# Kernel tuning notes

Hardware: AMD Instinct MI355X
Metric: run time of the kernel (lower is better)

Reference implementation:

```python
import jax, jax.numpy as jnp
import numpy as np

N_S, N_T, E = 50000, 50000, 600000
D_IN, D_H, D_OUT = 256, 128, 64


def setup_inputs() -> dict:
    key = jax.random.key(0)
    k1, k2, k3, k4, k5, k6 = jax.random.split(key, 6)
    edge_src = jax.random.randint(k1, (E,), 0, N_S, dtype=jnp.int32)
    edge_dst = jax.random.randint(k2, (E,), 0, N_T, dtype=jnp.int32)
    edge_index = jnp.stack([edge_src, edge_dst], axis=0)  # [2, E]
    x_s = jax.random.normal(k3, (N_S, D_IN), dtype=jnp.float32)
    x_t = jax.random.normal(k4, (N_T, D_IN), dtype=jnp.float32)
    W0 = jax.random.normal(k5, (D_IN, D_H), dtype=jnp.float32) * (1.0 / np.sqrt(D_IN))
    W1 = jax.random.normal(k6, (D_H, D_OUT), dtype=jnp.float32) * (1.0 / np.sqrt(D_H))
    return {"edge_index": edge_index, "x_s": x_s, "x_t": x_t, "W0": W0, "W1": W1}


def gcn_conv(x, src, dst, W):
    """PyG GCNConv, bias=False: D^{-1/2}(A+I)D^{-1/2} (x @ W)."""
    N = x.shape[0]
    h = x @ W  # [N, out]
    loops = jnp.arange(N, dtype=src.dtype)
    s = jnp.concatenate([src, loops])  # add self-loops
    d = jnp.concatenate([dst, loops])
    deg = jax.ops.segment_sum(jnp.ones_like(d, dtype=h.dtype), d, num_segments=N)
    dinv = jnp.where(deg > 0, jax.lax.rsqrt(deg), 0.0)
    norm = dinv[s] * dinv[d]  # [E+N]
    return jax.ops.segment_sum(h[s] * norm[:, None], d, num_segments=N)


def reference(edge_index, x_s, x_t, W0, W1):
    n_s = x_s.shape[0]
    src = edge_index[0]
    dst = edge_index[1] + n_s  # targets live in the x_t block
    acts = [jax.nn.relu, lambda v: v]
    Ws = [W0, W1]
    for W, act in zip(Ws, acts):
        x = jnp.concatenate([x_s, x_t], axis=0)
        x = act(gcn_conv(x, src, dst, W))
        x_s, x_t = x[:n_s], x[n_s:]
    return (x_s, x_t)
```

## Files before the change

kernel.cpp:

```cpp
#include <hip/hip_runtime.h>
#include <cstdint>
#include <cstddef>

typedef unsigned short u16;
typedef unsigned int   u32;
typedef __attribute__((ext_vector_type(8))) short bf16x8;
typedef __attribute__((ext_vector_type(4))) float f32x4;

#define D_IN  256
#define D_H   128
#define D_OUT 64
#define LSTR  72

__device__ __forceinline__ float bf2f(u16 u){
  union { u32 i; float f; } v; v.i = ((u32)u) << 16; return v.f;
}
__device__ __forceinline__ u16 f2bf(float f){
  union { float f; u32 i; } v; v.f = f;
  u32 r = (v.i + 0x7fffu + ((v.i >> 16) & 1u)) >> 16;
  return (u16)r;
}

__global__ void k_wprep(const float* __restrict__ W0, const float* __restrict__ W1,
                        u16* __restrict__ W0t, u16* __restrict__ W1t,
                        int* __restrict__ deg, int n_t){
  int i = blockIdx.x * 256 + threadIdx.x;
  if (i < 128 * 256){
    int n = i >> 8, k = i & 255;
    W0t[i] = f2bf(W0[(size_t)k * 128 + n]);
  } else if (i < 128 * 256 + 64 * 128){
    int j = i - 128 * 256;
    int n = j >> 7, k = j & 127;
    W1t[j] = f2bf(W1[(size_t)k * 64 + n]);
  } else if (i - (128 * 256 + 64 * 128) < n_t){
    deg[i - (128 * 256 + 64 * 128)] = 0;
  }
}

__global__ void k_deg(const int* __restrict__ dst, int E, int* __restrict__ deg){
  int e = blockIdx.x * 256 + threadIdx.x;
  if (e < E) atomicAdd(&deg[dst[e]], 1);
}

__global__ __launch_bounds__(256) void k_bsum(const int* __restrict__ deg, int N,
                                              int* __restrict__ bsum){
  __shared__ int s[256];
  int tid = threadIdx.x;
  int i = blockIdx.x * 256 + tid;
  s[tid] = (i < N) ? deg[i] : 0;
  __syncthreads();
  for (int o = 128; o > 0; o >>= 1){
    if (tid < o) s[tid] += s[tid + o];
    __syncthreads();
  }
  if (tid == 0) bsum[blockIdx.x] = s[0];
}

__global__ __launch_bounds__(256) void k_off(const int* __restrict__ deg, int N,
                                             const int* __restrict__ bsum, int nb,
                                             int* __restrict__ off, int* __restrict__ cursor,
                                             float* __restrict__ dinv){
  __shared__ int s[256];
  __shared__ int sbase[256];
  const int tid = threadIdx.x;
  const int bid = blockIdx.x;
  const int i   = bid * 256 + tid;
  int acc = 0;
  for (int j = tid; j < bid; j += 256) acc += bsum[j];
  sbase[tid] = acc;
  int v = (i < N) ? deg[i] : 0;
  s[tid] = v;
  __syncthreads();
  for (int o = 128; o > 0; o >>= 1){
    if (tid < o) sbase[tid] += sbase[tid + o];
    __syncthreads();
  }
  for (int o = 1; o < 256; o <<= 1){
    int t = (tid >= o) ? s[tid - o] : 0;
    __syncthreads();
    s[tid] += t;
    __syncthreads();
  }
  if (i < N){
    int excl = s[tid] - v + sbase[0];
    off[i] = excl;
    cursor[i] = excl;
    dinv[i] = rsqrtf((float)v + 1.0f);
  }
}

__global__ void k_fill(const int* __restrict__ src, const int* __restrict__ dst,
                       int E, int* __restrict__ cursor, int* __restrict__ csr){
  int e = blockIdx.x * 256 + threadIdx.x;
  if (e < E){
    int d = dst[e];
    int p = atomicAdd(&cursor[d], 1);
    csr[p] = src[e];
  }
}

__global__ __launch_bounds__(256) void k_gemm1(
    const float* __restrict__ Xs, const float* __restrict__ Xt,
    const u16* __restrict__ W0t, int M, int n_s,
    u16* __restrict__ out)
{
  __shared__ u16 As[128 * LSTR];
  __shared__ u16 Bs[128 * LSTR];
  const int t    = threadIdx.x;
  const int wave = t >> 6, lane = t & 63;
  const int wm   = (wave >> 1) * 64, wn = (wave & 1) * 64;
  const int lm   = lane & 15, quad = lane >> 4;
  const int row0 = blockIdx.x * 128;

  f32x4 acc[4][4];
  const f32x4 z = {0.f, 0.f, 0.f, 0.f};
  #pragma unroll
  for (int i = 0; i < 4; i++)
    #pragma unroll
    for (int j = 0; j < 4; j++) acc[i][j] = z;

  const int ar = t >> 1;
  const int kh = (t & 1) * 32;
  const int r  = row0 + ar;
  const float* xp = nullptr;
  if (r < M) xp = (r < n_s) ? (Xs + (size_t)r * D_IN) : (Xt + (size_t)(r - n_s) * D_IN);
  const u16* wrow = W0t + (size_t)ar * D_IN + kh;

  float4 a4[8];
  int4   b4[4];
  if (xp){
    #pragma unroll
    for (int j = 0; j < 8; j++) a4[j] = *(const float4*)(xp + kh + j * 4);
  } else {
    float4 zz = make_float4(0,0,0,0);
    #pragma unroll
    for (int j = 0; j < 8; j++) a4[j] = zz;
  }
  #pragma unroll
  for (int j = 0; j < 4; j++) b4[j] = *(const int4*)(wrow + j * 8);

  for (int k0 = 0; k0 < D_IN; k0 += 64){
    __syncthreads();
    {
      u16 abuf[32];
      #pragma unroll
      for (int j = 0; j < 8; j++){
        abuf[j*4+0] = f2bf(a4[j].x); abuf[j*4+1] = f2bf(a4[j].y);
        abuf[j*4+2] = f2bf(a4[j].z); abuf[j*4+3] = f2bf(a4[j].w);
      }
      u16* ap = &As[ar * LSTR + kh];
      *(int4*)(ap +  0) = *(int4*)&abuf[0];
      *(int4*)(ap +  8) = *(int4*)&abuf[8];
      *(int4*)(ap + 16) = *(int4*)&abuf[16];
      *(int4*)(ap + 24) = *(int4*)&abuf[24];
      u16* bp = &Bs[ar * LSTR + kh];
      *(int4*)(bp +  0) = b4[0];
      *(int4*)(bp +  8) = b4[1];
      *(int4*)(bp + 16) = b4[2];
      *(int4*)(bp + 24) = b4[3];
    }
    __syncthreads();

    if (k0 + 64 < D_IN){
      if (xp){
        #pragma unroll
        for (int j = 0; j < 8; j++) a4[j] = *(const float4*)(xp + k0 + 64 + kh + j * 4);
      }
      #pragma unroll
      for (int j = 0; j < 4; j++) b4[j] = *(const int4*)(wrow + k0 + 64 + j * 8);
    }

    #pragma unroll
    for (int kk = 0; kk < 64; kk += 32){
      bf16x8 af[4], bfr[4];
      #pragma unroll
      for (int i = 0; i < 4; i++)
        af[i] = *(const bf16x8*)&As[(wm + i*16 + lm) * LSTR + kk + quad*8];
      #pragma unroll
      for (int i = 0; i < 4; i++)
        bfr[i] = *(const bf16x8*)&Bs[(wn + i*16 + lm) * LSTR + kk + quad*8];
      #pragma unroll
      for (int mi = 0; mi < 4; mi++)
        #pragma unroll
        for (int ni = 0; ni < 4; ni++)
          acc[mi][ni] = __builtin_amdgcn_mfma_f32_16x16x32_bf16(
              af[mi], bfr[ni], acc[mi][ni], 0, 0, 0);
    }
  }

  #pragma unroll
  for (int mi = 0; mi < 4; mi++){
    int rbase = row0 + wm + mi * 16 + quad * 4;
    #pragma unroll
    for (int rr = 0; rr < 4; rr++){
      int m = rbase + rr;
      if (m >= M) continue;
      u16* op = out + (size_t)m * D_H + wn + lm;
      #pragma unroll
      for (int ni = 0; ni < 4; ni++)
        op[ni * 16] = f2bf(acc[mi][ni][rr]);
    }
  }
}

__global__ __launch_bounds__(256) void k_aggf(
    const int* __restrict__ off, const int* __restrict__ deg,
    const int* __restrict__ csr, const float* __restrict__ dinv,
    u16* __restrict__ h1, int n_s, int n_t)
{
  int w    = (blockIdx.x * 256 + threadIdx.x) >> 6;
  int lane = threadIdx.x & 63;
  if (w >= n_t) return;
  const int g = lane >> 4;
  const int c = lane & 15;
  int start = off[w];
  int n     = deg[w];

  float r[8], p[8];
  #pragma unroll
  for (int q = 0; q < 8; q++){ r[q] = 0.f; p[q] = 0.f; }

  int i = 0;
  for (; i + 8 <= n; i += 8){
    int sa = csr[start + i + g];
    int sb = csr[start + i + 4 + g];
    int4 da = *(const int4*)(h1 + (size_t)sa * D_H + c * 8);
    int4 db = *(const int4*)(h1 + (size_t)sb * D_H + c * 8);
    const u16* ha = (const u16*)&da;
    const u16* hb = (const u16*)&db;
    #pragma unroll
    for (int q = 0; q < 8; q++){
      float va = bf2f(ha[q]), vb = bf2f(hb[q]);
      r[q] += va + vb;
      p[q] += fmaxf(va, 0.f) + fmaxf(vb, 0.f);
    }
  }
  for (; i < n; i += 4){
    if (i + g < n){
      int sa = csr[start + i + g];
      int4 da = *(const int4*)(h1 + (size_t)sa * D_H + c * 8);
      const u16* ha = (const u16*)&da;
      #pragma unroll
      for (int q = 0; q < 8; q++){
        float va = bf2f(ha[q]);
        r[q] += va;
        p[q] += fmaxf(va, 0.f);
      }
    }
  }

  #pragma unroll
  for (int q = 0; q < 8; q++){
    r[q] += __shfl_xor(r[q], 16, 64);
    r[q] += __shfl_xor(r[q], 32, 64);
    p[q] += __shfl_xor(p[q], 16, 64);
    p[q] += __shfl_xor(p[q], 32, 64);
  }

  if (g == 0){
    float di  = dinv[w];
    float di2 = di * di;
    u16* selfp = h1 + (size_t)(n_s + w) * D_H + c * 8;
    int4 hs = *(const int4*)selfp;
    const u16* hh = (const u16*)&hs;
    u16 ob[8];
    #pragma unroll
    for (int q = 0; q < 8; q++){
      float zq = fmaxf(di * r[q] + di2 * bf2f(hh[q]), 0.f);
      float uq = di * p[q] + di2 * zq;
      ob[q] = f2bf(uq);
    }
    *(int4*)selfp = *(int4*)ob;
  }
}

__global__ __launch_bounds__(256) void k_gemm2(
    const u16* __restrict__ h1, const u16* __restrict__ W1t,
    int M, int n_s, float* __restrict__ out)
{
  __shared__ u16 As[128 * LSTR];
  __shared__ u16 Bs[64 * LSTR];
  const int t    = threadIdx.x;
  const int wave = t >> 6, lane = t & 63;
  const int wm   = wave * 32;
  const int lm   = lane & 15, quad = lane >> 4;
  const int row0 = blockIdx.x * 128;

  f32x4 acc[2][4];
  const f32x4 z = {0.f, 0.f, 0.f, 0.f};
  #pragma unroll
  for (int i = 0; i < 2; i++)
    #pragma unroll
    for (int j = 0; j < 4; j++) acc[i][j] = z;

  const int ar = t >> 1;
  const int kh = (t & 1) * 32;
  const int r  = row0 + ar;
  const bool relu_a = (r < n_s);
  const int bn = t >> 2;
  const int bk = (t & 3) * 16;

  int4 a4[4], w4[2];
  if (r < M){
    const u16* hp = h1 + (size_t)r * D_H + kh;
    #pragma unroll
    for (int j = 0; j < 4; j++) a4[j] = *(const int4*)(hp + j * 8);
  } else {
    int4 zz = make_int4(0,0,0,0);
    #pragma unroll
    for (int j = 0; j < 4; j++) a4[j] = zz;
  }
  w4[0] = *(const int4*)(W1t + (size_t)bn * D_H + bk);
  w4[1] = *(const int4*)(W1t + (size_t)bn * D_H + bk + 8);

  for (int k0 = 0; k0 < D_H; k0 += 64){
    __syncthreads();
    {
      u16 abuf[32];
      #pragma unroll
      for (int j = 0; j < 4; j++){
        u16* hh = (u16*)&a4[j];
        #pragma unroll
        for (int q = 0; q < 8; q++){
          u16 v = hh[q];
          abuf[j*8+q] = (relu_a && (v & 0x8000u)) ? (u16)0 : v;
        }
      }
      u16* ap = &As[ar * LSTR + kh];
      *(int4*)(ap +  0) = *(int4*)&abuf[0];
      *(int4*)(ap +  8) = *(int4*)&abuf[8];
      *(int4*)(ap + 16) = *(int4*)&abuf[16];
      *(int4*)(ap + 24) = *(int4*)&abuf[24];
      u16* bp = &Bs[bn * LSTR + bk];
      *(int4*)(bp + 0) = w4[0];
      *(int4*)(bp + 8) = w4[1];
    }
    __syncthreads();

    if (k0 + 64 < D_H){
      if (r < M){
        const u16* hp = h1 + (size_t)r * D_H + k0 + 64 + kh;
        #pragma unroll
        for (int j = 0; j < 4; j++) a4[j] = *(const int4*)(hp + j * 8);
      }
      w4[0] = *(const int4*)(W1t + (size_t)bn * D_H + k0 + 64 + bk);
      w4[1] = *(const int4*)(W1t + (size_t)bn * D_H + k0 + 64 + bk + 8);
    }

    #pragma unroll
    for (int kk = 0; kk < 64; kk += 32){
      bf16x8 af[2], bfr[4];
      #pragma unroll
      for (int i = 0; i < 2; i++)
        af[i] = *(const bf16x8*)&As[(wm + i*16 + lm) * LSTR + kk + quad*8];
      #pragma unroll
      for (int i = 0; i < 4; i++)
        bfr[i] = *(const bf16x8*)&Bs[(i*16 + lm) * LSTR + kk + quad*8];
      #pragma unroll
      for (int mi = 0; mi < 2; mi++)
        #pragma unroll
        for (int ni = 0; ni < 4; ni++)
          acc[mi][ni] = __builtin_amdgcn_mfma_f32_16x16x32_bf16(
              af[mi], bfr[ni], acc[mi][ni], 0, 0, 0);
    }
  }

  #pragma unroll
  for (int mi = 0; mi < 2; mi++){
    int rbase = row0 + wm + mi * 16 + quad * 4;
    #pragma unroll
    for (int rr = 0; rr < 4; rr++){
      int m = rbase + rr;
      if (m >= M) continue;
      float* op = out + (size_t)m * D_OUT + lm;
      #pragma unroll
      for (int ni = 0; ni < 4; ni++)
        op[ni * 16] = acc[mi][ni][rr];
    }
  }
}

static inline size_t alup(size_t x){ return (x + 255) & ~(size_t)255; }

extern "C" void kernel_launch(void* const* d_in, const int* in_sizes, int n_in,
                              void* d_out, int out_size, void* d_ws, size_t ws_size,
                              hipStream_t stream)
{
  const int*   ei = (const int*)d_in[0];
  const float* xs = (const float*)d_in[1];
  const float* xt = (const float*)d_in[2];
  const float* W0 = (const float*)d_in[3];
  const float* W1 = (const float*)d_in[4];
  const int E   = in_sizes[0] / 2;
  const int n_s = in_sizes[1] / D_IN;
  const int n_t = in_sizes[2] / D_IN;
  const int M   = n_s + n_t;
  const int* src = ei;
  const int* dst = ei + E;
  const int nb_t = (n_t + 255) / 256;

  char* p = (char*)d_ws;
  int*   deg    = (int*)p;    p += alup((size_t)n_t * 4);
  int*   off    = (int*)p;    p += alup((size_t)n_t * 4);
  int*   cursor = (int*)p;    p += alup((size_t)n_t * 4);
  float* dinv   = (float*)p;  p += alup((size_t)n_t * 4);
  int*   bsum   = (int*)p;    p += alup((size_t)nb_t * 4);
  int*   csr    = (int*)p;    p += alup((size_t)E * 4);
  u16*   W0t    = (u16*)p;    p += alup((size_t)D_H * D_IN * 2);
  u16*   W1t    = (u16*)p;    p += alup((size_t)D_OUT * D_H * 2);
  u16*   h1     = (u16*)p;    p += alup((size_t)M * D_H * 2);

  const int wprep_n = 128*256 + 64*128 + n_t;
  k_wprep <<<(wprep_n + 255) / 256, 256, 0, stream>>>(W0, W1, W0t, W1t, deg, n_t);
  k_deg   <<<(E + 255) / 256, 256, 0, stream>>>(dst, E, deg);
  k_bsum  <<<nb_t, 256, 0, stream>>>(deg, n_t, bsum);
  k_off   <<<nb_t, 256, 0, stream>>>(deg, n_t, bsum, nb_t, off, cursor, dinv);
  k_fill  <<<(E + 255) / 256, 256, 0, stream>>>(src, dst, E, cursor, csr);

  k_gemm1<<<(M + 127) / 128, 256, 0, stream>>>(xs, xt, W0t, M, n_s, h1);
  k_aggf <<<(n_t + 3) / 4, 256, 0, stream>>>(off, deg, csr, dinv, h1, n_s, n_t);
  k_gemm2<<<(M + 127) / 128, 256, 0, stream>>>(h1, W1t, M, n_s, (float*)d_out);
}
```

Before: 279.5 us.

## Drop LDS staging in both GEMMs; load MFMA fragments directly from global

Both dense GEMM kernels stop staging tiles through shared memory with __syncthreads barriers. Each wave now owns 32 rows and loads its A and B MFMA fragments straight from global memory into registers, with register double-buffering across K steps. This removes the LDS traffic and barriers, but each wave now re-reads the whole weight matrix from global or cache, and A-row loads become strided per lane rather than coalesced.

Result: no change. 280.6 us (+0.4%).

```diff
diff --git a/kernel.cpp b/kernel.cpp
--- a/kernel.cpp
+++ b/kernel.cpp
@@ -10,7 +10,6 @@
 #define D_IN  256
 #define D_H   128
 #define D_OUT 64
-#define LSTR  72
 
 __device__ __forceinline__ float bf2f(u16 u){
   union { u32 i; float f; } v; v.i = ((u32)u) << 16; return v.f;
@@ -104,101 +103,80 @@
     const u16* __restrict__ W0t, int M, int n_s,
     u16* __restrict__ out)
 {
-  __shared__ u16 As[128 * LSTR];
-  __shared__ u16 Bs[128 * LSTR];
   const int t    = threadIdx.x;
   const int wave = t >> 6, lane = t & 63;
-  const int wm   = (wave >> 1) * 64, wn = (wave & 1) * 64;
   const int lm   = lane & 15, quad = lane >> 4;
-  const int row0 = blockIdx.x * 128;
-
-  f32x4 acc[4][4];
+  const int rowW = blockIdx.x * 128 + wave * 32;
+
+  const float* pa0;
+  const float* pa1;
+  {
+    int r0 = rowW + lm;       int c0 = (r0 < M) ? r0 : 0;
+    int r1 = rowW + 16 + lm;  int c1 = (r1 < M) ? r1 : 0;
+    pa0 = ((c0 < n_s) ? (Xs + (size_t)c0 * D_IN) : (Xt + (size_t)(c0 - n_s) * D_IN)) + quad * 8;
+    pa1 = ((c1 < n_s) ? (Xs + (size_t)c1 * D_IN) : (Xt + (size_t)(c1 - n_s) * D_IN)) + quad * 8;
+  }
+  const u16* pb = W0t + (size_t)lm * D_IN + quad * 8;
+
+  f32x4 acc[2][8];
   const f32x4 z = {0.f, 0.f, 0.f, 0.f};
   #pragma unroll
-  for (int i = 0; i < 4; i++)
-    #pragma unroll
-    for (int j = 0; j < 4; j++) acc[i][j] = z;
-
-  const int ar = t >> 1;
-  const int kh = (t & 1) * 32;
-  const int r  = row0 + ar;
-  const float* xp = nullptr;
-  if (r < M) xp = (r < n_s) ? (Xs + (size_t)r * D_IN) : (Xt + (size_t)(r - n_s) * D_IN);
-  const u16* wrow = W0t + (size_t)ar * D_IN + kh;
-
-  float4 a4[8];
-  int4   b4[4];
-  if (xp){
-    #pragma unroll
-    for (int j = 0; j < 8; j++) a4[j] = *(const float4*)(xp + kh + j * 4);
-  } else {
-    float4 zz = make_float4(0,0,0,0);
-    #pragma unroll
-    for (int j = 0; j < 8; j++) a4[j] = zz;
-  }
-  #pragma unroll
-  for (int j = 0; j < 4; j++) b4[j] = *(const int4*)(wrow + j * 8);
-
-  for (int k0 = 0; k0 < D_IN; k0 += 64){
-    __syncthreads();
-    {
-      u16 abuf[32];
-      #pragma unroll
-      for (int j = 0; j < 8; j++){
-        abuf[j*4+0] = f2bf(a4[j].x); abuf[j*4+1] = f2bf(a4[j].y);
-        abuf[j*4+2] = f2bf(a4[j].z); abuf[j*4+3] = f2bf(a4[j].w);
-      }
-      u16* ap = &As[ar * LSTR + kh];
-      *(int4*)(ap +  0) = *(int4*)&abuf[0];
-      *(int4*)(ap +  8) = *(int4*)&abuf[8];
-      *(int4*)(ap + 16) = *(int4*)&abuf[16];
-      *(int4*)(ap + 24) = *(int4*)&abuf[24];
-      u16* bp = &Bs[ar * LSTR + kh];
-      *(int4*)(bp +  0) = b4[0];
-      *(int4*)(bp +  8) = b4[1];
-      *(int4*)(bp + 16) = b4[2];
-      *(int4*)(bp + 24) = b4[3];
-    }
-    __syncthreads();
-
-    if (k0 + 64 < D_IN){
-      if (xp){
-        #pragma unroll
-        for (int j = 0; j < 8; j++) a4[j] = *(const float4*)(xp + k0 + 64 + kh + j * 4);
-      }
-      #pragma unroll
-      for (int j = 0; j < 4; j++) b4[j] = *(const int4*)(wrow + k0 + 64 + j * 8);
-    }
-
-    #pragma unroll
-    for (int kk = 0; kk < 64; kk += 32){
-      bf16x8 af[4], bfr[4];
-      #pragma unroll
-      for (int i = 0; i < 4; i++)
-        af[i] = *(const bf16x8*)&As[(wm + i*16 + lm) * LSTR + kk + quad*8];
-      #pragma unroll
-      for (int i = 0; i < 4; i++)
-        bfr[i] = *(const bf16x8*)&Bs[(wn + i*16 + lm) * LSTR + kk + quad*8];
-      #pragma unroll
-      for (int mi = 0; mi < 4; mi++)
-        #pragma unroll
-        for (int ni = 0; ni < 4; ni++)
-          acc[mi][ni] = __builtin_amdgcn_mfma_f32_16x16x32_bf16(
-              af[mi], bfr[ni], acc[mi][ni], 0, 0, 0);
-    }
-  }
-
-  #pragma unroll
-  for (int mi = 0; mi < 4; mi++){
-    int rbase = row0 + wm + mi * 16 + quad * 4;
+  for (int i = 0; i < 2; i++)
+    #pragma unroll
+    for (int j = 0; j < 8; j++) acc[i][j] = z;
+
+  float4 a[2][4];
+  int4   b[2][8];
+
+  a[0][0] = *(const float4*)(pa0);
+  a[0][1] = *(const float4*)(pa0 + 4);
+  a[0][2] = *(const float4*)(pa1);
+  a[0][3] = *(const float4*)(pa1 + 4);
+  #pragma unroll
+  for (int nf = 0; nf < 8; nf++)
+    b[0][nf] = *(const int4*)(pb + (size_t)nf * 16 * D_IN);
+
+  #pragma unroll
+  for (int kk = 0; kk < 8; kk++){
+    const int cur = kk & 1, nxt = cur ^ 1;
+    if (kk < 7){
+      const int ko = (kk + 1) * 32;
+      a[nxt][0] = *(const float4*)(pa0 + ko);
+      a[nxt][1] = *(const float4*)(pa0 + ko + 4);
+      a[nxt][2] = *(const float4*)(pa1 + ko);
+      a[nxt][3] = *(const float4*)(pa1 + ko + 4);
+      #pragma unroll
+      for (int nf = 0; nf < 8; nf++)
+        b[nxt][nf] = *(const int4*)(pb + (size_t)nf * 16 * D_IN + ko);
+    }
+    bf16x8 af[2];
+    #pragma unroll
+    for (int mi = 0; mi < 2; mi++){
+      const float* fa = (const float*)&a[cur][mi * 2];
+      u16 tmp[8];
+      #pragma unroll
+      for (int q = 0; q < 8; q++) tmp[q] = f2bf(fa[q]);
+      af[mi] = *(const bf16x8*)tmp;
+    }
+    #pragma unroll
+    for (int mi = 0; mi < 2; mi++)
+      #pragma unroll
+      for (int nf = 0; nf < 8; nf++)
+        acc[mi][nf] = __builtin_amdgcn_mfma_f32_16x16x32_bf16(
+            af[mi], *(const bf16x8*)&b[cur][nf], acc[mi][nf], 0, 0, 0);
+  }
+
+  #pragma unroll
+  for (int mi = 0; mi < 2; mi++){
+    int rbase = rowW + mi * 16 + quad * 4;
     #pragma unroll
     for (int rr = 0; rr < 4; rr++){
       int m = rbase + rr;
       if (m >= M) continue;
-      u16* op = out + (size_t)m * D_H + wn + lm;
-      #pragma unroll
-      for (int ni = 0; ni < 4; ni++)
-        op[ni * 16] = f2bf(acc[mi][ni][rr]);
+      u16* op = out + (size_t)m * D_H + lm;
+      #pragma unroll
+      for (int nf = 0; nf < 8; nf++)
+        op[nf * 16] = f2bf(acc[mi][nf][rr]);
     }
   }
 }
@@ -274,17 +252,32 @@
   }
 }
 
+__device__ __forceinline__ bf16x8 relu_bf(int4 v, bool relu){
+  const u16* s = (const u16*)&v;
+  u16 tmp[8];
+  #pragma unroll
+  for (int q = 0; q < 8; q++){
+    u16 x = s[q];
+    tmp[q] = (relu && (x & 0x8000u)) ? (u16)0 : x;
+  }
+  return *(const bf16x8*)tmp;
+}
+
 __global__ __launch_bounds__(256) void k_gemm2(
     const u16* __restrict__ h1, const u16* __restrict__ W1t,
     int M, int n_s, float* __restrict__ out)
 {
-  __shared__ u16 As[128 * LSTR];
-  __shared__ u16 Bs[64 * LSTR];
   const int t    = threadIdx.x;
   const int wave = t >> 6, lane = t & 63;
-  const int wm   = wave * 32;
   const int lm   = lane & 15, quad = lane >> 4;
-  const int row0 = blockIdx.x * 128;
+  const int rowW = blockIdx.x * 128 + wave * 32;
+
+  int r0 = rowW + lm, r1 = rowW + 16 + lm;
+  const bool relu0 = (r0 < n_s), relu1 = (r1 < n_s);
+  int c0 = (r0 < M) ? r0 : 0, c1 = (r1 < M) ? r1 : 0;
+  const u16* pa0 = h1 + (size_t)c0 * D_H + quad * 8;
+  const u16* pa1 = h1 + (size_t)c1 * D_H + quad * 8;
+  const u16* pb  = W1t + (size_t)lm * D_H + quad * 8;
 
   f32x4 acc[2][4];
   const f32x4 z = {0.f, 0.f, 0.f, 0.f};
@@ -293,89 +286,46 @@
     #pragma unroll
     for (int j = 0; j < 4; j++) acc[i][j] = z;
 
-  const int ar = t >> 1;
-  const int kh = (t & 1) * 32;
-  const int r  = row0 + ar;
-  const bool relu_a = (r < n_s);
-  const int bn = t >> 2;
-  const int bk = (t & 3) * 16;
-
-  int4 a4[4], w4[2];
-  if (r < M){
-    const u16* hp = h1 + (size_t)r * D_H + kh;
-    #pragma unroll
-    for (int j = 0; j < 4; j++) a4[j] = *(const int4*)(hp + j * 8);
-  } else {
-    int4 zz = make_int4(0,0,0,0);
-    #pragma unroll
-    for (int j = 0; j < 4; j++) a4[j] = zz;
-  }
-  w4[0] = *(const int4*)(W1t + (size_t)bn * D_H + bk);
-  w4[1] = *(const int4*)(W1t + (size_t)bn * D_H + bk + 8);
-
-  for (int k0 = 0; k0 < D_H; k0 += 64){
-    __syncthreads();
-    {
-      u16 abuf[32];
-      #pragma unroll
-      for (int j = 0; j < 4; j++){
-        u16* hh = (u16*)&a4[j];
-        #pragma unroll
-        for (int q = 0; q < 8; q++){
-          u16 v = hh[q];
-          abuf[j*8+q] = (relu_a && (v & 0x8000u)) ? (u16)0 : v;
-        }
-      }
-      u16* ap = &As[ar * LSTR + kh];
-      *(int4*)(ap +  0) = *(int4*)&abuf[0];
-      *(int4*)(ap +  8) = *(int4*)&abuf[8];
-      *(int4*)(ap + 16) = *(int4*)&abuf[16];
-      *(int4*)(ap + 24) = *(int4*)&abuf[24];
-      u16* bp = &Bs[bn * LSTR + bk];
-      *(int4*)(bp + 0) = w4[0];
-      *(int4*)(bp + 8) = w4[1];
-    }
-    __syncthreads();
-
-    if (k0 + 64 < D_H){
-      if (r < M){
-        const u16* hp = h1 + (size_t)r * D_H + k0 + 64 + kh;
-        #pragma unroll
-        for (int j = 0; j < 4; j++) a4[j] = *(const int4*)(hp + j * 8);
-      }
-      w4[0] = *(const int4*)(W1t + (size_t)bn * D_H + k0 + 64 + bk);
-      w4[1] = *(const int4*)(W1t + (size_t)bn * D_H + k0 + 64 + bk + 8);
-    }
-
-    #pragma unroll
-    for (int kk = 0; kk < 64; kk += 32){
-      bf16x8 af[2], bfr[4];
-      #pragma unroll
-      for (int i = 0; i < 2; i++)
-        af[i] = *(const bf16x8*)&As[(wm + i*16 + lm) * LSTR + kk + quad*8];
-      #pragma unroll
-      for (int i = 0; i < 4; i++)
-        bfr[i] = *(const bf16x8*)&Bs[(i*16 + lm) * LSTR + kk + quad*8];
-      #pragma unroll
-      for (int mi = 0; mi < 2; mi++)
-        #pragma unroll
-        for (int ni = 0; ni < 4; ni++)
-          acc[mi][ni] = __builtin_amdgcn_mfma_f32_16x16x32_bf16(
-              af[mi], bfr[ni], acc[mi][ni], 0, 0, 0);
-    }
+  int4 a[2][2], b[2][4];
+  a[0][0] = *(const int4*)(pa0);
+  a[0][1] = *(const int4*)(pa1);
+  #pragma unroll
+  for (int nf = 0; nf < 4; nf++)
+    b[0][nf] = *(const int4*)(pb + (size_t)nf * 16 * D_H);
+
+  #pragma unroll
+  for (int kk = 0; kk < 4; kk++){
+    const int cur = kk & 1, nxt = cur ^ 1;
+    if (kk < 3){
+      const int ko = (kk + 1) * 32;
+      a[nxt][0] = *(const int4*)(pa0 + ko);
+      a[nxt][1] = *(const int4*)(pa1 + ko);
+      #pragma unroll
+      for (int nf = 0; nf < 4; nf++)
+        b[nxt][nf] = *(const int4*)(pb + (size_t)nf * 16 * D_H + ko);
+    }
+    bf16x8 af[2];
+    af[0] = relu_bf(a[cur][0], relu0);
+    af[1] = relu_bf(a[cur][1], relu1);
+    #pragma unroll
+    for (int mi = 0; mi < 2; mi++)
+      #pragma unroll
+      for (int nf = 0; nf < 4; nf++)
+        acc[mi][nf] = __builtin_amdgcn_mfma_f32_16x16x32_bf16(
+            af[mi], *(const bf16x8*)&b[cur][nf], acc[mi][nf], 0, 0, 0);
   }
 
   #pragma unroll
   for (int mi = 0; mi < 2; mi++){
-    int rbase = row0 + wm + mi * 16 + quad * 4;
+    int rbase = rowW + mi * 16 + quad * 4;
     #pragma unroll
     for (int rr = 0; rr < 4; rr++){
       int m = rbase + rr;
       if (m >= M) continue;
       float* op = out + (size_t)m * D_OUT + lm;
       #pragma unroll
-      for (int ni = 0; ni < 4; ni++)
-        op[ni * 16] = acc[mi][ni][rr];
+      for (int nf = 0; nf < 4; nf++)
+        op[nf * 16] = acc[mi][nf][rr];
     }
   }
 }
```
